# Optimization experiments

Hardware: AMD Instinct MI355X
Metric: run time of the kernel (lower is better)

The kernel has to match this reference:

```python
import jax, jax.numpy as jnp
import numpy as np

N, E, G = 20000, 320000, 64
IN_DIM, HID, HEADS, NCLS = 512, 256, 2, 10
EPS = 1e-5
SLOPE = 0.2


def setup_inputs() -> dict:
    key = jax.random.key(0)
    ks = jax.random.split(key, 24)
    s = 0.02
    inp = {
        "feat": jax.random.normal(ks[0], (N, IN_DIM), jnp.float32),
        "src": jax.random.randint(ks[1], (E,), 0, N, jnp.int32),
        "dst": jax.random.randint(ks[2], (E,), 0, N, jnp.int32),
        "graph_ids": jnp.sort(jax.random.randint(ks[3], (N,), 0, G, jnp.int32)),
        # GATv2Conv params (fc_src, fc_dst, attn)
        "W_src": jax.random.normal(ks[4], (IN_DIM, HEADS * HID), jnp.float32) * s,
        "b_src": jnp.zeros((HEADS * HID,), jnp.float32),
        "W_dst": jax.random.normal(ks[5], (IN_DIM, HEADS * HID), jnp.float32) * s,
        "b_dst": jnp.zeros((HEADS * HID,), jnp.float32),
        "attn": jax.random.normal(ks[6], (HEADS, HID), jnp.float32) * s,
        # skip_lin: input_dim -> 2*hidden
        "W_skip": jax.random.normal(ks[7], (IN_DIM, 2 * HID), jnp.float32) * s,
        "b_skip": jnp.zeros((2 * HID,), jnp.float32),
        # bn1 affine
        "gamma": jnp.ones((2 * HID,), jnp.float32),
        "beta": jnp.zeros((2 * HID,), jnp.float32),
        # dim_reducer
        "W_red": jax.random.normal(ks[8], (2 * HID, HID), jnp.float32) * s,
        "b_red": jnp.zeros((HID,), jnp.float32),
        # attention-pool gate Linear(hidden, 1)
        "w_gate": jax.random.normal(ks[9], (HID, 1), jnp.float32) * s,
        "b_gate": jnp.zeros((1,), jnp.float32),
        # classifier MLP
        "W1": jax.random.normal(ks[10], (HID, HID // 2), jnp.float32) * s,
        "b1": jnp.zeros((HID // 2,), jnp.float32),
        "W2": jax.random.normal(ks[11], (HID // 2, NCLS), jnp.float32) * s,
        "b2": jnp.zeros((NCLS,), jnp.float32),
    }
    return inp


def _gatv2(feat, src, dst, W_src, b_src, W_dst, b_dst, attn):
    # feat_src/feat_dst: [N, H, D]
    fs = (feat @ W_src + b_src).reshape(N, HEADS, HID)
    fd = (feat @ W_dst + b_dst).reshape(N, HEADS, HID)
    fs_e = fs[src]                               # [E, H, D]
    m = jax.nn.leaky_relu(fs_e + fd[dst], SLOPE)  # [E, H, D]
    e = jnp.einsum("ehd,hd->eh", m, attn)         # [E, H]
    # edge softmax grouped by destination node
    e_max = jax.ops.segment_max(e, dst, num_segments=N)          # [N, H]
    e_exp = jnp.exp(e - e_max[dst])                               # [E, H]
    denom = jax.ops.segment_sum(e_exp, dst, num_segments=N)      # [N, H]
    alpha = e_exp / denom[dst]                                    # [E, H]
    out = jax.ops.segment_sum(alpha[:, :, None] * fs_e, dst, num_segments=N)
    return out  # [N, H, D]; zero rows for zero in-degree nodes


def reference(feat, src, dst, graph_ids, W_src, b_src, W_dst, b_dst, attn,
              W_skip, b_skip, gamma, beta, W_red, b_red, w_gate, b_gate,
              W1, b1, W2, b2):
    h1 = jax.nn.elu(_gatv2(feat, src, dst, W_src, b_src, W_dst, b_dst, attn))
    h1 = h1.reshape(N, HEADS * HID)
    h1 = h1 + (feat @ W_skip + b_skip)
    # BatchNorm1d (training-mode batch statistics, biased variance)
    mu = jnp.mean(h1, axis=0)
    var = jnp.mean((h1 - mu) ** 2, axis=0)
    h1 = (h1 - mu) * jax.lax.rsqrt(var + EPS) * gamma + beta
    hr = h1 @ W_red + b_red                      # [N, HID]
    # GlobalAttentionPooling: segment softmax of gate scores over each graph
    gate = hr @ w_gate + b_gate                  # [N, 1]
    g_max = jax.ops.segment_max(gate, graph_ids, num_segments=G)
    g_exp = jnp.exp(gate - g_max[graph_ids])
    g_den = jax.ops.segment_sum(g_exp, graph_ids, num_segments=G)
    a = g_exp / g_den[graph_ids]                 # [N, 1]
    h_g = jax.ops.segment_sum(a * hr, graph_ids, num_segments=G)  # [G, HID]
    # classifier (dropout = identity at inference)
    return jax.nn.relu(h_g @ W1 + b1) @ W2 + b2  # [G, NCLS]
```

## Files before the change

### kernel.cpp

```cpp
#include <hip/hip_runtime.h>
#include <math.h>

#define N_NODES 20000
#define N_EDGES 320000
#define N_GRAPH 64
#define IN_DIM  512
#define HID     256
#define F2      512
#define EPS_BN  1e-5f
#define SLOPE   0.2f
#define SCAN_BLOCKS 79
#define N_RT    157
#define RT_PAD  20096

#define SF_BLOCKS   5024
#define SW_BLOCKS   1024
#define INIT_BLOCKS 79
#define HIST_BLOCKS 1250
#define PREP_BLOCKS (SF_BLOCKS + SW_BLOCKS + INIT_BLOCKS + HIST_BLOCKS)
#define TRIPLE_BLOCKS 1920

typedef unsigned short u16;
typedef __attribute__((ext_vector_type(8))) short bf16x8;
typedef __attribute__((ext_vector_type(4))) float floatx4;
typedef _Float16 f16;
typedef __attribute__((ext_vector_type(2))) f16 f16x2;

__device__ __forceinline__ u16 bf_hi(float x) {
    unsigned int u = __float_as_uint(x);
    return (u16)((u + 0x7fffu + ((u >> 16) & 1u)) >> 16);
}
__device__ __forceinline__ float bf_val(u16 h) {
    return __uint_as_float((unsigned int)h << 16);
}
__device__ __forceinline__ f16x2 h2_from_u32(unsigned int u) {
    return __builtin_bit_cast(f16x2, u);
}
__device__ __forceinline__ unsigned int u32_from_h2(f16x2 h) {
    return __builtin_bit_cast(unsigned int, h);
}

__device__ __forceinline__ void gload16(const u16* g, u16* l) {
    __builtin_amdgcn_global_load_lds(
        (const __attribute__((address_space(1))) void*)g,
        (__attribute__((address_space(3))) void*)l, 16, 0, 0);
}

__global__ __launch_bounds__(256) void prep_kernel(
    const float* __restrict__ feat, u16* __restrict__ Fhi,
    const float* __restrict__ Ws, const float* __restrict__ Wd,
    const float* __restrict__ Wk, const float* __restrict__ Wr,
    u16* __restrict__ Whi, u16* __restrict__ Wlo,
    const int* __restrict__ dst, int* __restrict__ counts,
    int* __restrict__ cursor,
    float* __restrict__ stats, float* __restrict__ h_gnum,
    float* __restrict__ gden, float* __restrict__ gate) {
    __shared__ float t[32][33];
    int b = blockIdx.x;
    int tid = threadIdx.x;
    if (b < SF_BLOCKS) {
        int i = b * 256 + tid;
        size_t base = (size_t)i * 8;
        if (i >= N_NODES * IN_DIM / 8) {
            *(uint4*)(Fhi + base) = make_uint4(0, 0, 0, 0);
            return;
        }
        float4 x0 = *(const float4*)(feat + base);
        float4 x1 = *(const float4*)(feat + base + 4);
        float xs[8] = {x0.x, x0.y, x0.z, x0.w, x1.x, x1.y, x1.z, x1.w};
        union { u16 s[8]; uint4 v; } h;
#pragma unroll
        for (int j = 0; j < 8; j++) h.s[j] = bf_hi(xs[j]);
        *(uint4*)(Fhi + base) = h.v;
    } else if (b < SF_BLOCKS + SW_BLOCKS) {
        int bb = b - SF_BLOCKS;
        int kx = bb & 15, ny = (bb >> 4) & 15, w = bb >> 8;
        int ncols = (w == 3) ? 256 : 512;
        int n0 = ny * 32;
        if (n0 >= ncols) return;
        const float* W = (w == 0) ? Ws : ((w == 1) ? Wd : ((w == 2) ? Wk : Wr));
        size_t obase = (size_t)w * 512 * 512;
        int k0 = kx * 32;
        int tx = tid & 31, ty = tid >> 5;
#pragma unroll
        for (int i = 0; i < 4; i++)
            t[ty * 4 + i][tx] = W[(size_t)(k0 + ty * 4 + i) * ncols + n0 + tx];
        __syncthreads();
#pragma unroll
        for (int i = 0; i < 4; i++) {
            float x = t[tx][ty * 4 + i];
            u16 hh = bf_hi(x);
            size_t o = obase + (size_t)(n0 + ty * 4 + i) * 512 + k0 + tx;
            Whi[o] = hh;
            Wlo[o] = bf_hi(x - bf_val(hh));
        }
    } else if (b < SF_BLOCKS + SW_BLOCKS + INIT_BLOCKS) {
        int i = (b - SF_BLOCKS - SW_BLOCKS) * 256 + tid;
        if (i < N_NODES) { cursor[i] = 0; gate[i] = 0.f; }
        if (i < 1024) stats[i] = 0.f;
        if (i < N_GRAPH * HID) h_gnum[i] = 0.f;
        if (i < N_GRAPH) gden[i] = 0.f;
    } else {
        int e = (b - SF_BLOCKS - SW_BLOCKS - INIT_BLOCKS) * 256 + tid;
        if (e < N_EDGES) atomicAdd(&counts[dst[e]], 1);
    }
}

__global__ __launch_bounds__(256) void gemm_mfma_triple(
    const u16* __restrict__ Fhi, const u16* __restrict__ Wthi,
    const float* __restrict__ b_src, const float* __restrict__ b_dst,
    const float* __restrict__ b_skip,
    u16* __restrict__ FS16, u16* __restrict__ FD16,
    u16* __restrict__ h1hi, u16* __restrict__ h1lo,
    const int* __restrict__ counts, int* __restrict__ row_ptr,
    int* __restrict__ bsum) {
    __shared__ u16 S[2][2][8192];
    int b = blockIdx.x;
    int tid = threadIdx.x;
    if (b >= TRIPLE_BLOCKS) {
        int* buf = (int*)&S[0][0][0];
        int bb = b - TRIPLE_BLOCKS;
        int i = bb * 256 + tid;
        buf[tid] = (i < N_NODES) ? counts[i] : 0;
        __syncthreads();
        for (int off = 1; off < 256; off <<= 1) {
            int t = (tid >= off) ? buf[tid - off] : 0;
            __syncthreads();
            buf[tid] += t;
            __syncthreads();
        }
        if (i < N_NODES) row_ptr[i + 1] = buf[tid];
        if (tid == 255) bsum[bb] = buf[255];
        return;
    }
    int xcd = b & 7, slot = b >> 3;
    int rt = (slot / 12) * 8 + xcd;
    if (rt >= N_RT) return;
    int cw = slot % 12;
    int w_idx = cw >> 2;
    int col0 = (cw & 3) * 128;
    int row0 = rt * 128;
    int lane = tid & 63, wave = tid >> 6;
    int wm = (wave & 1) * 64, wn = (wave >> 1) * 64;
    int quad = lane >> 4, l16 = lane & 15;

    int lrow = lane >> 3;
    int kswz = ((lane & 7) ^ lrow) << 3;
    const u16* aS = Fhi + (size_t)(row0 + wave * 32 + lrow) * 512 + kswz;
    const u16* bS = Wthi + (size_t)w_idx * 512 * 512 +
                    (size_t)(col0 + wave * 32 + lrow) * 512 + kswz;

#define STAGE(buf, kk)                                                        \
    do {                                                                      \
        gload16(aS + (size_t)(kk) * 64,         &S[buf][0][(wave * 4 + 0) * 512]); \
        gload16(bS + (size_t)(kk) * 64,         &S[buf][1][(wave * 4 + 0) * 512]); \
        gload16(aS + 4096 + (size_t)(kk) * 64,  &S[buf][0][(wave * 4 + 1) * 512]); \
        gload16(bS + 4096 + (size_t)(kk) * 64,  &S[buf][1][(wave * 4 + 1) * 512]); \
        gload16(aS + 8192 + (size_t)(kk) * 64,  &S[buf][0][(wave * 4 + 2) * 512]); \
        gload16(bS + 8192 + (size_t)(kk) * 64,  &S[buf][1][(wave * 4 + 2) * 512]); \
        gload16(aS + 12288 + (size_t)(kk) * 64, &S[buf][0][(wave * 4 + 3) * 512]); \
        gload16(bS + 12288 + (size_t)(kk) * 64, &S[buf][1][(wave * 4 + 3) * 512]); \
    } while (0)

    int kx8 = (l16 & 7) << 3;
    int oS0 = (quad * 8) ^ kx8;
    int offA = (wm + l16) * 64;
    int offB = (wn + l16) * 64;

    floatx4 acc[4][4];
#pragma unroll
    for (int i = 0; i < 4; i++)
#pragma unroll
        for (int j = 0; j < 4; j++) acc[i][j] = (floatx4){0.f, 0.f, 0.f, 0.f};

    STAGE(0, 0);
    __syncthreads();

#pragma unroll
    for (int kk = 0; kk < 8; kk++) {
        if (kk < 7) STAGE((kk + 1) & 1, kk + 1);
        const u16* A = &S[kk & 1][0][0];
        const u16* B = &S[kk & 1][1][0];
        bf16x8 bv[4][2];
#pragma unroll
        for (int nt = 0; nt < 4; nt++) {
            bv[nt][0] = *(const bf16x8*)&B[offB + nt * 1024 + oS0];
            bv[nt][1] = *(const bf16x8*)&B[offB + nt * 1024 + (oS0 ^ 32)];
        }
#pragma unroll
        for (int mt = 0; mt < 4; mt++) {
            bf16x8 a0 = *(const bf16x8*)&A[offA + mt * 1024 + oS0];
            bf16x8 a1 = *(const bf16x8*)&A[offA + mt * 1024 + (oS0 ^ 32)];
#pragma unroll
            for (int nt = 0; nt < 4; nt++) {
                acc[mt][nt] = __builtin_amdgcn_mfma_f32_16x16x32_bf16(
                    bv[nt][0], a0, acc[mt][nt], 0, 0, 0);
                acc[mt][nt] = __builtin_amdgcn_mfma_f32_16x16x32_bf16(
                    bv[nt][1], a1, acc[mt][nt], 0, 0, 0);
            }
        }
        __syncthreads();
    }
#undef STAGE

    const float* bias = (w_idx == 0) ? b_src : ((w_idx == 1) ? b_dst : b_skip);
    float4 b4[4];
#pragma unroll
    for (int wt = 0; wt < 4; wt++)
        b4[wt] = *(const float4*)(bias + col0 + wn + wt * 16 + quad * 4);

    u16* C = &S[0][0][0];
#pragma unroll
    for (int ft = 0; ft < 4; ft++) {
        int r = wm + ft * 16 + l16;
        int rx = r & 7;
#pragma unroll
        for (int wt = 0; wt < 4; wt++) {
            int cb = wn + wt * 16 + quad * 4;
            int off = r * 128 + (((cb >> 3) ^ rx) << 3) + (cb & 4);
            float v0 = acc[ft][wt][0] + b4[wt].x;
            float v1 = acc[ft][wt][1] + b4[wt].y;
            float v2 = acc[ft][wt][2] + b4[wt].z;
            float v3 = acc[ft][wt][3] + b4[wt].w;
            if (w_idx <= 1) {
                f16x2 p0; p0[0] = (f16)v0; p0[1] = (f16)v1;
                f16x2 p1; p1[0] = (f16)v2; p1[1] = (f16)v3;
                uint2 wv;
                wv.x = u32_from_h2(p0);
                wv.y = u32_from_h2(p1);
                *(uint2*)&C[off] = wv;
            } else {
                u16 h0 = bf_hi(v0), h1_ = bf_hi(v1), h2 = bf_hi(v2), h3 = bf_hi(v3);
                uint2 wv;
                wv.x = (unsigned)h0 | ((unsigned)h1_ << 16);
                wv.y = (unsigned)h2 | ((unsigned)h3 << 16);
                *(uint2*)&C[off] = wv;
                uint2 lv;
                lv.x = (unsigned)bf_hi(v0 - bf_val(h0)) | ((unsigned)bf_hi(v1 - bf_val(h1_)) << 16);
                lv.y = (unsigned)bf_hi(v2 - bf_val(h2)) | ((unsigned)bf_hi(v3 - bf_val(h3)) << 16);
                *(uint2*)&C[16384 + off] = lv;
            }
        }
    }
    __syncthreads();
    {
        int tr = tid >> 4;
        int tc = tid & 15;
        u16* outp = (w_idx == 0) ? FS16 : ((w_idx == 1) ? FD16 : h1hi);
#pragma unroll
        for (int i = 0; i < 8; i++) {
            int r = i * 16 + tr;
            int m = row0 + r;
            int loff = r * 128 + ((tc ^ (r & 7)) << 3);
            uint4 v = *(const uint4*)&C[loff];
            if (m < N_NODES) {
                *(uint4*)(outp + (size_t)m * 512 + col0 + tc * 8) = v;
                if (w_idx == 2) {
                    uint4 vl = *(const uint4*)&C[16384 + loff];
                    *(uint4*)(h1lo + (size_t)m * 512 + col0 + tc * 8) = vl;
                }
            }
        }
    }
}

__global__ __launch_bounds__(256) void scan_fixup_kernel(
    const int* __restrict__ bsum, int* __restrict__ row_ptr) {
    __shared__ int red[256];
    int b = blockIdx.x, tid = threadIdx.x;
    red[tid] = (tid < b) ? bsum[tid] : 0;
    __syncthreads();
    for (int off = 128; off > 0; off >>= 1) {
        if (tid < off) red[tid] += red[tid + off];
        __syncthreads();
    }
    int offset = red[0];
    int i = b * 256 + tid;
    if (i < N_NODES) row_ptr[i + 1] += offset;
    if (b == 0 && tid == 0) row_ptr[0] = 0;
}

__global__ void scatter_kernel(const int* __restrict__ src, const int* __restrict__ dst,
                               const int* __restrict__ row_ptr,
                               int* __restrict__ cursor, int* __restrict__ csr_src) {
    int e = blockIdx.x * blockDim.x + threadIdx.x;
    if (e < N_EDGES) {
        int d = dst[e];
        int pos = atomicAdd(&cursor[d], 1);
        csr_src[row_ptr[d] + pos] = src[e];
    }
}

__global__ __launch_bounds__(128) void edge_fused_kernel(
    const u16* __restrict__ FS16, const u16* __restrict__ FD16,
    const float* __restrict__ attn, const int* __restrict__ csr_src,
    const int* __restrict__ row_ptr,
    u16* __restrict__ h1hi, u16* __restrict__ h1lo) {
    int tid = threadIdx.x;
    int lane = tid & 63, wave = tid >> 6;
    int n = blockIdx.x * 2 + wave;
    int beg = row_ptr[n], end = row_ptr[n + 1];

    f16x2 fd2[4], aw2[4];
    {
        uint4 q = *(const uint4*)(FD16 + (size_t)n * 512 + 8 * lane);
        fd2[0] = h2_from_u32(q.x); fd2[1] = h2_from_u32(q.y);
        fd2[2] = h2_from_u32(q.z); fd2[3] = h2_from_u32(q.w);
        float4 a0 = *(const float4*)(attn + 8 * lane);
        float4 a1 = *(const float4*)(attn + 8 * lane + 4);
        aw2[0][0] = (f16)a0.x; aw2[0][1] = (f16)a0.y;
        aw2[1][0] = (f16)a0.z; aw2[1][1] = (f16)a0.w;
        aw2[2][0] = (f16)a1.x; aw2[2][1] = (f16)a1.y;
        aw2[3][0] = (f16)a1.z; aw2[3][1] = (f16)a1.w;
    }

    const f16x2 sl2 = {(f16)SLOPE, (f16)SLOPE};
    float acc[8] = {0.f, 0.f, 0.f, 0.f, 0.f, 0.f, 0.f, 0.f};
    float den = 0.f;
    const u16* FSb = FS16 + 8 * lane;

    int j = beg;
    for (; j + 3 < end; j += 4) {
        int s0 = csr_src[j];
        int s1 = csr_src[j + 1];
        int s2 = csr_src[j + 2];
        int s3 = csr_src[j + 3];
        uint4 q0 = *(const uint4*)(FSb + (size_t)s0 * 512);
        uint4 q1 = *(const uint4*)(FSb + (size_t)s1 * 512);
        uint4 q2 = *(const uint4*)(FSb + (size_t)s2 * 512);
        uint4 q3 = *(const uint4*)(FSb + (size_t)s3 * 512);
        f16x2 f0[4], f1[4], f2[4], f3[4];
        f0[0] = h2_from_u32(q0.x); f0[1] = h2_from_u32(q0.y);
        f0[2] = h2_from_u32(q0.z); f0[3] = h2_from_u32(q0.w);
        f1[0] = h2_from_u32(q1.x); f1[1] = h2_from_u32(q1.y);
        f1[2] = h2_from_u32(q1.z); f1[3] = h2_from_u32(q1.w);
        f2[0] = h2_from_u32(q2.x); f2[1] = h2_from_u32(q2.y);
        f2[2] = h2_from_u32(q2.z); f2[3] = h2_from_u32(q2.w);
        f3[0] = h2_from_u32(q3.x); f3[1] = h2_from_u32(q3.y);
        f3[2] = h2_from_u32(q3.z); f3[3] = h2_from_u32(q3.w);
        float p0 = 0.f, p1 = 0.f, p2 = 0.f, p3 = 0.f;
#pragma unroll
        for (int k = 0; k < 4; k++) {
            f16x2 sm0 = f0[k] + fd2[k];
            p0 = __builtin_amdgcn_fdot2(
                __builtin_elementwise_max(sm0, sm0 * sl2), aw2[k], p0, false);
            f16x2 sm1 = f1[k] + fd2[k];
            p1 = __builtin_amdgcn_fdot2(
                __builtin_elementwise_max(sm1, sm1 * sl2), aw2[k], p1, false);
            f16x2 sm2 = f2[k] + fd2[k];
            p2 = __builtin_amdgcn_fdot2(
                __builtin_elementwise_max(sm2, sm2 * sl2), aw2[k], p2, false);
            f16x2 sm3 = f3[k] + fd2[k];
            p3 = __builtin_amdgcn_fdot2(
                __builtin_elementwise_max(sm3, sm3 * sl2), aw2[k], p3, false);
        }
#pragma unroll
        for (int off = 16; off > 0; off >>= 1) {
            p0 += __shfl_xor(p0, off, 64);
            p1 += __shfl_xor(p1, off, 64);
            p2 += __shfl_xor(p2, off, 64);
            p3 += __shfl_xor(p3, off, 64);
        }
        float e0 = __expf(p0);
        float e1 = __expf(p1);
        float e2 = __expf(p2);
        float e3 = __expf(p3);
#pragma unroll
        for (int k = 0; k < 4; k++) {
            acc[2 * k]     += e0 * (float)f0[k][0] + e1 * (float)f1[k][0]
                            + e2 * (float)f2[k][0] + e3 * (float)f3[k][0];
            acc[2 * k + 1] += e0 * (float)f0[k][1] + e1 * (float)f1[k][1]
                            + e2 * (float)f2[k][1] + e3 * (float)f3[k][1];
        }
        den += (e0 + e1) + (e2 + e3);
    }
    for (; j < end; j++) {
        int s = csr_src[j];
        uint4 q = *(const uint4*)(FSb + (size_t)s * 512);
        f16x2 f2v[4];
        f2v[0] = h2_from_u32(q.x); f2v[1] = h2_from_u32(q.y);
        f2v[2] = h2_from_u32(q.z); f2v[3] = h2_from_u32(q.w);
        float p = 0.f;
#pragma unroll
        for (int k = 0; k < 4; k++) {
            f16x2 sm = f2v[k] + fd2[k];
            p = __builtin_amdgcn_fdot2(
                __builtin_elementwise_max(sm, sm * sl2), aw2[k], p, false);
        }
#pragma unroll
        for (int off = 16; off > 0; off >>= 1) p += __shfl_xor(p, off, 64);
        float ex = __expf(p);
#pragma unroll
        for (int k = 0; k < 4; k++) {
            acc[2 * k]     += ex * (float)f2v[k][0];
            acc[2 * k + 1] += ex * (float)f2v[k][1];
        }
        den += ex;
    }

    float inv = den > 0.f ? 1.f / den : 0.f;
    size_t base = (size_t)n * 512 + 8 * lane;
    union { u16 s[8]; uint4 v; } qh, ql;
    qh.v = *(const uint4*)(h1hi + base);
    ql.v = *(const uint4*)(h1lo + base);
#pragma unroll
    for (int k = 0; k < 8; k++) {
        float skip = bf_val(qh.s[k]) + bf_val(ql.s[k]);
        float x = acc[k] * inv;
        x = x > 0.f ? x : expm1f(x);
        float y = x + skip;
        u16 hh = bf_hi(y);
        qh.s[k] = hh;
        ql.s[k] = bf_hi(y - bf_val(hh));
    }
    *(uint4*)(h1hi + base) = qh.v;
    *(uint4*)(h1lo + base) = ql.v;
}

__global__ __launch_bounds__(256) void bn_stats_kernel(const u16* __restrict__ h1hi,
                                                       float* __restrict__ stats,
                                                       int rows_per_block) {
    int tid = threadIdx.x;
    int r0 = blockIdx.x * rows_per_block;
    int r1 = min(r0 + rows_per_block, N_NODES);
    float s0 = 0.f, q0 = 0.f, s1 = 0.f, q1 = 0.f;
    for (int r = r0; r < r1; r++) {
        float a = bf_val(h1hi[(size_t)r * F2 + tid]);
        float b = bf_val(h1hi[(size_t)r * F2 + 256 + tid]);
        s0 += a; q0 += a * a;
        s1 += b; q1 += b * b;
    }
    atomicAdd(&stats[tid], s0);
    atomicAdd(&stats[256 + tid], s1);
    atomicAdd(&stats[512 + tid], q0);
    atomicAdd(&stats[512 + 256 + tid], q1);
}

__global__ __launch_bounds__(256) void bn_fold_kernel(
    const float* __restrict__ stats, const float* __restrict__ gamma,
    const float* __restrict__ beta,
    const u16* __restrict__ Whi3, const u16* __restrict__ Wlo3,
    const float* __restrict__ b_red,
    u16* __restrict__ Wphi, u16* __restrict__ Wplo, float* __restrict__ bias2) {
    __shared__ float sScale[512], sShift[512];
    __shared__ float red[256];
    int n = blockIdx.x, tid = threadIdx.x;
    for (int c = tid; c < 512; c += 256) {
        float mu = stats[c] / (float)N_NODES;
        float var = stats[512 + c] / (float)N_NODES - mu * mu;
        float sc = gamma[c] * rsqrtf(var + EPS_BN);
        sScale[c] = sc;
        sShift[c] = beta[c] - mu * sc;
    }
    __syncthreads();
    float part = 0.f;
    for (int k = tid; k < 512; k += 256) {
        size_t o = (size_t)n * 512 + k;
        float w = bf_val(Whi3[o]) + bf_val(Wlo3[o]);
        part += sShift[k] * w;
        float wp = w * sScale[k];
        u16 hh = bf_hi(wp);
        Wphi[o] = hh;
        Wplo[o] = bf_hi(wp - bf_val(hh));
    }
    red[tid] = part; __syncthreads();
    for (int off = 128; off > 0; off >>= 1) {
        if (tid < off) red[tid] += red[tid + off];
        __syncthreads();
    }
    if (tid == 0) bias2[n] = b_red[n] + red[0];
}

__global__ __launch_bounds__(256) void gemm_mfma_red(
    const u16* __restrict__ Ahi, const u16* __restrict__ Alo,
    const u16* __restrict__ Bhi, const u16* __restrict__ Blo,
    const float* __restrict__ bias2, const float* __restrict__ wg,
    float* __restrict__ hr, float* __restrict__ gate) {
    __shared__ float CS[128 * 128];
    u16* AsHi = (u16*)CS;
    u16* AsLo = (u16*)CS + 128 * 40;
    int tid = threadIdx.x;
    int row0 = blockIdx.x * 128;
    int col0 = blockIdx.y * 128;
    int lane = tid & 63, wave = tid >> 6;
    int wm = (wave & 1) * 64, wn = (wave >> 1) * 64;
    int quad = lane >> 4, l16 = lane & 15;

    int sr = tid >> 1, sh = (tid & 1) * 16;
    int grow = row0 + sr;
    bool ok = grow < N_NODES;
    u16* sH = &AsHi[sr * 40 + sh];
    u16* sL = &AsLo[sr * 40 + sh];

    const u16* bPh[4];
    const u16* bPl[4];
#pragma unroll
    for (int nt = 0; nt < 4; nt++) {
        size_t o = (size_t)(col0 + wn + nt * 16 + l16) * 512 + quad * 8;
        bPh[nt] = Bhi + o;
        bPl[nt] = Blo + o;
    }

    floatx4 acc[4][4];
#pragma unroll
    for (int i = 0; i < 4; i++)
#pragma unroll
        for (int j = 0; j < 4; j++) acc[i][j] = (floatx4){0.f, 0.f, 0.f, 0.f};

    for (int k0 = 0; k0 < 512; k0 += 32) {
        uint4 h0 = make_uint4(0, 0, 0, 0), h1v = h0, l0 = h0, l1 = h0;
        if (ok) {
            const u16* g = Ahi + (size_t)grow * 512 + k0 + sh;
            const u16* gl = Alo + (size_t)grow * 512 + k0 + sh;
            h0 = *(const uint4*)(g);
            h1v = *(const uint4*)(g + 8);
            l0 = *(const uint4*)(gl);
            l1 = *(const uint4*)(gl + 8);
        }
        union { uint4 u; bf16x8 v; } bh[4], bl[4];
#pragma unroll
        for (int nt = 0; nt < 4; nt++) {
            bh[nt].u = *(const uint4*)(bPh[nt] + k0);
            bl[nt].u = *(const uint4*)(bPl[nt] + k0);
        }
        __syncthreads();
        *(uint4*)(sH + 0) = h0;
        *(uint4*)(sH + 8) = h1v;
        *(uint4*)(sL + 0) = l0;
        *(uint4*)(sL + 8) = l1;
        __syncthreads();
#pragma unroll
        for (int mt = 0; mt < 4; mt++) {
            int me = (wm + mt * 16 + l16) * 40 + quad * 8;
            bf16x8 ah = *(const bf16x8*)&AsHi[me];
            bf16x8 al = *(const bf16x8*)&AsLo[me];
#pragma unroll
            for (int nt = 0; nt < 4; nt++) {
                acc[mt][nt] = __builtin_amdgcn_mfma_f32_16x16x32_bf16(bh[nt].v, ah, acc[mt][nt], 0, 0, 0);
                acc[mt][nt] = __builtin_amdgcn_mfma_f32_16x16x32_bf16(bl[nt].v, ah, acc[mt][nt], 0, 0, 0);
                acc[mt][nt] = __builtin_amdgcn_mfma_f32_16x16x32_bf16(bh[nt].v, al, acc[mt][nt], 0, 0, 0);
            }
        }
    }
    __syncthreads();

    float4 b4[4], w4[4];
#pragma unroll
    for (int wt = 0; wt < 4; wt++) {
        int nb = col0 + wn + wt * 16 + quad * 4;
        b4[wt] = *(const float4*)(bias2 + nb);
        w4[wt] = *(const float4*)(wg + nb);
    }
#pragma unroll
    for (int ft = 0; ft < 4; ft++) {
        int r = wm + ft * 16 + l16;
        int m = row0 + r;
        bool ok2 = m < N_NODES;
        float g = 0.f;
#pragma unroll
        for (int wt = 0; wt < 4; wt++) {
            int cb = wn + wt * 16 + quad * 4;
            float4 v;
            v.x = acc[ft][wt][0] + b4[wt].x;
            v.y = acc[ft][wt][1] + b4[wt].y;
            v.z = acc[ft][wt][2] + b4[wt].z;
            v.w = acc[ft][wt][3] + b4[wt].w;
            g += v.x * w4[wt].x + v.y * w4[wt].y + v.z * w4[wt].z + v.w * w4[wt].w;
            *(float4*)&CS[r * 128 + (((cb >> 2) ^ (r & 7)) << 2)] = v;
        }
        g += __shfl_xor(g, 16, 64);
        g += __shfl_xor(g, 32, 64);
        if (ok2 && lane < 16) atomicAdd(&gate[m], g);
    }
    __syncthreads();
    {
        int trr = tid >> 5;
        int tc = tid & 31;
#pragma unroll
        for (int it = 0; it < 16; it++) {
            int r = it * 8 + trr;
            int m = row0 + r;
            if (m < N_NODES) {
                float4 v = *(const float4*)&CS[r * 128 + ((tc ^ (r & 7)) << 2)];
                *(float4*)(hr + (size_t)m * HID + col0 + tc * 4) = v;
            }
        }
    }
}

__device__ __forceinline__ int lower_bound_dev(const int* a, int n, int v) {
    int lo = 0, hi = n;
    while (lo < hi) {
        int mid = (lo + hi) >> 1;
        if (a[mid] < v) lo = mid + 1; else hi = mid;
    }
    return lo;
}

__global__ __launch_bounds__(256) void pool_partial_kernel(
    const float* __restrict__ hr, const float* __restrict__ gate,
    const int* __restrict__ gids, float* __restrict__ h_gnum,
    float* __restrict__ gden) {
    int b = blockIdx.x;
    int g = b >> 3, part = b & 7;
    int tid = threadIdx.x;
    int start = lower_bound_dev(gids, N_NODES, g);
    int end = lower_bound_dev(gids, N_NODES, g + 1);
    int span = end - start;
    int p_beg = start + (span * part) / 8;
    int p_end = start + (span * (part + 1)) / 8;
    if (p_beg >= p_end) return;
    __shared__ float wa[256];
    __shared__ float red[256];
    float acc = 0.f, denacc = 0.f;
    for (int cbeg = p_beg; cbeg < p_end; cbeg += 256) {
        int c = min(256, p_end - cbeg);
        float e = 0.f;
        if (tid < c) { e = expf(gate[cbeg + tid]); wa[tid] = e; }
        red[tid] = (tid < c) ? e : 0.f;
        __syncthreads();
        for (int off = 128; off > 0; off >>= 1) {
            if (tid < off) red[tid] += red[tid + off];
            __syncthreads();
        }
        denacc += red[0];
        for (int i = 0; i < c; i++) acc += wa[i] * hr[(size_t)(cbeg + i) * HID + tid];
        __syncthreads();
    }
    atomicAdd(&h_gnum[g * HID + tid], acc);
    if (tid == 0) atomicAdd(&gden[g], denacc);
}

__global__ __launch_bounds__(128) void classifier_kernel(
    const float* __restrict__ h_gnum, const float* __restrict__ gden,
    const float* __restrict__ W1, const float* __restrict__ b1,
    const float* __restrict__ W2, const float* __restrict__ b2,
    float* __restrict__ out) {
    int g = blockIdx.x;
    int tid = threadIdx.x;
    __shared__ float hg[256];
    __shared__ float z1[128];
    float d = gden[g];
    float invd = d > 0.f ? 1.f / d : 0.f;
    hg[tid] = h_gnum[g * HID + tid] * invd;
    hg[tid + 128] = h_gnum[g * HID + tid + 128] * invd;
    __syncthreads();
    float a = b1[tid];
#pragma unroll 8
    for (int k = 0; k < 256; k++) a += hg[k] * W1[k * 128 + tid];
    z1[tid] = a > 0.f ? a : 0.f;
    __syncthreads();
    if (tid < 10) {
        float o = b2[tid];
#pragma unroll 8
        for (int j = 0; j < 128; j++) o += z1[j] * W2[j * 10 + tid];
        out[g * 10 + tid] = o;
    }
}

extern "C" void kernel_launch(void* const* d_in, const int* in_sizes, int n_in,
                              void* d_out, int out_size, void* d_ws, size_t ws_size,
                              hipStream_t stream) {
    const float* feat   = (const float*)d_in[0];
    const int*   src    = (const int*)d_in[1];
    const int*   dst    = (const int*)d_in[2];
    const int*   gids   = (const int*)d_in[3];
    const float* W_src  = (const float*)d_in[4];
    const float* b_src  = (const float*)d_in[5];
    const float* W_dst  = (const float*)d_in[6];
    const float* b_dst  = (const float*)d_in[7];
    const float* attn   = (const float*)d_in[8];
    const float* W_skip = (const float*)d_in[9];
    const float* b_skip = (const float*)d_in[10];
    const float* gamma  = (const float*)d_in[11];
    const float* beta   = (const float*)d_in[12];
    const float* W_red  = (const float*)d_in[13];
    const float* b_red  = (const float*)d_in[14];
    const float* w_gate = (const float*)d_in[15];
    const float* W1     = (const float*)d_in[17];
    const float* b1     = (const float*)d_in[18];
    const float* W2     = (const float*)d_in[19];
    const float* b2     = (const float*)d_in[20];
    float* out = (float*)d_out;

    char* p = (char*)d_ws;
    auto alloc = [&](size_t bytes) -> char* {
        char* r = p;
        p += (bytes + 255) & ~(size_t)255;
        return r;
    };
    u16*   FS16     = (u16*)alloc((size_t)N_NODES * F2 * 2);
    u16*   FD16     = (u16*)alloc((size_t)N_NODES * F2 * 2);
    u16*   h1hi     = (u16*)alloc((size_t)N_NODES * F2 * 2);
    u16*   h1lo     = (u16*)alloc((size_t)N_NODES * F2 * 2);
    float* gate     = (float*)alloc((size_t)N_NODES * 4);
    float* stats    = (float*)alloc(1024 * 4);
    float* bias2    = (float*)alloc(256 * 4);
    float* h_gnum   = (float*)alloc((size_t)N_GRAPH * HID * 4);
    float* gden     = (float*)alloc((size_t)N_GRAPH * 4);
    int* counts     = (int*)alloc((size_t)N_NODES * 4);
    int* row_ptr    = (int*)alloc((size_t)(N_NODES + 1) * 4);
    int* cursor     = (int*)alloc((size_t)N_NODES * 4);
    int* csr_src    = (int*)alloc((size_t)N_EDGES * 4);
    int* bsum       = (int*)alloc((size_t)SCAN_BLOCKS * 4);
    u16* Fhi        = (u16*)alloc((size_t)RT_PAD * IN_DIM * 2);
    u16* Wthi       = (u16*)alloc((size_t)4 * 512 * 512 * 2);
    u16* Wtlo       = (u16*)alloc((size_t)4 * 512 * 512 * 2);
    u16* Wphi       = (u16*)alloc((size_t)HID * 512 * 2);
    u16* Wplo       = (u16*)alloc((size_t)HID * 512 * 2);
    float* hr = (float*)Fhi;
    (void)ws_size; (void)in_sizes; (void)n_in; (void)out_size;

    const size_t WSZ = (size_t)512 * 512;

    hipMemsetAsync(counts, 0, (size_t)N_NODES * 4, stream);

    prep_kernel<<<PREP_BLOCKS, 256, 0, stream>>>(
        feat, Fhi, W_src, W_dst, W_skip, W_red, Wthi, Wtlo,
        dst, counts, cursor, stats, h_gnum, gden, gate);

    gemm_mfma_triple<<<TRIPLE_BLOCKS + SCAN_BLOCKS, 256, 0, stream>>>(
        Fhi, Wthi, b_src, b_dst, b_skip, FS16, FD16, h1hi, h1lo,
        counts, row_ptr, bsum);

    scan_fixup_kernel<<<SCAN_BLOCKS, 256, 0, stream>>>(bsum, row_ptr);
    scatter_kernel<<<(N_EDGES + 255) / 256, 256, 0, stream>>>(src, dst, row_ptr, cursor, csr_src);

    edge_fused_kernel<<<N_NODES / 2, 128, 0, stream>>>(
        FS16, FD16, attn, csr_src, row_ptr, h1hi, h1lo);

    bn_stats_kernel<<<500, 256, 0, stream>>>(h1hi, stats, 40);
    bn_fold_kernel<<<HID, 256, 0, stream>>>(
        stats, gamma, beta, Wthi + 3 * WSZ, Wtlo + 3 * WSZ, b_red, Wphi, Wplo, bias2);

    dim3 g256((N_NODES + 127) / 128, 2);
    gemm_mfma_red<<<g256, 256, 0, stream>>>(
        h1hi, h1lo, Wphi, Wplo, bias2, w_gate, hr, gate);

    pool_partial_kernel<<<N_GRAPH * 8, 256, 0, stream>>>(hr, gate, gids, h_gnum, gden);

    classifier_kernel<<<N_GRAPH, 128, 0, stream>>>(h_gnum, gden, W1, b1, W2, b2, out);
}
```

Measured before the change: 361.3 us.

## Fuse attention pooling into reduction GEMM epilogue and widen edge kernel blocks

The reduction GEMM now covers all 256 output columns in one 512-thread block per 128-row tile. It computes the gate score fully in shared memory, then accumulates exp(gate)-weighted rows into per-graph shared partial sums before flushing them to global memory with atomics. This removes the hr and gate intermediate arrays and the separate pool_partial kernel, which reread hr. The softmax max-subtraction is skipped, relying on gate values staying small, and the grid shrinks to 157 blocks, which may underfill the GPU. The edge kernel also moves from 2 to 4 waves per block.

```diff
diff --git a/kernel.cpp b/kernel.cpp
--- a/kernel.cpp
+++ b/kernel.cpp
@@ -54,7 +54,7 @@
     const int* __restrict__ dst, int* __restrict__ counts,
     int* __restrict__ cursor,
     float* __restrict__ stats, float* __restrict__ h_gnum,
-    float* __restrict__ gden, float* __restrict__ gate) {
+    float* __restrict__ gden) {
     __shared__ float t[32][33];
     int b = blockIdx.x;
     int tid = threadIdx.x;
@@ -96,7 +96,7 @@
         }
     } else if (b < SF_BLOCKS + SW_BLOCKS + INIT_BLOCKS) {
         int i = (b - SF_BLOCKS - SW_BLOCKS) * 256 + tid;
-        if (i < N_NODES) { cursor[i] = 0; gate[i] = 0.f; }
+        if (i < N_NODES) cursor[i] = 0;
         if (i < 1024) stats[i] = 0.f;
         if (i < N_GRAPH * HID) h_gnum[i] = 0.f;
         if (i < N_GRAPH) gden[i] = 0.f;
@@ -291,14 +291,14 @@
     }
 }
 
-__global__ __launch_bounds__(128) void edge_fused_kernel(
+__global__ __launch_bounds__(256) void edge_fused_kernel(
     const u16* __restrict__ FS16, const u16* __restrict__ FD16,
     const float* __restrict__ attn, const int* __restrict__ csr_src,
     const int* __restrict__ row_ptr,
     u16* __restrict__ h1hi, u16* __restrict__ h1lo) {
     int tid = threadIdx.x;
     int lane = tid & 63, wave = tid >> 6;
-    int n = blockIdx.x * 2 + wave;
+    int n = blockIdx.x * 4 + wave;
     int beg = row_ptr[n], end = row_ptr[n + 1];
 
     f16x2 fd2[4], aw2[4];
@@ -471,22 +471,28 @@
     if (tid == 0) bias2[n] = b_red[n] + red[0];
 }
 
-__global__ __launch_bounds__(256) void gemm_mfma_red(
+__global__ __launch_bounds__(512) void gemm_mfma_red(
     const u16* __restrict__ Ahi, const u16* __restrict__ Alo,
     const u16* __restrict__ Bhi, const u16* __restrict__ Blo,
     const float* __restrict__ bias2, const float* __restrict__ wg,
-    float* __restrict__ hr, float* __restrict__ gate) {
-    __shared__ float CS[128 * 128];
-    u16* AsHi = (u16*)CS;
-    u16* AsLo = (u16*)CS + 128 * 40;
+    const int* __restrict__ gids,
+    float* __restrict__ h_gnum, float* __restrict__ gden) {
+    __shared__ u16 AsHi[128 * 40];
+    __shared__ u16 AsLo[128 * 40];
+    __shared__ float gacc[128];
+    __shared__ float pacc[8][256];
+    __shared__ float dacc[8];
     int tid = threadIdx.x;
     int row0 = blockIdx.x * 128;
-    int col0 = blockIdx.y * 128;
     int lane = tid & 63, wave = tid >> 6;
     int wm = (wave & 1) * 64, wn = (wave >> 1) * 64;
     int quad = lane >> 4, l16 = lane & 15;
 
-    int sr = tid >> 1, sh = (tid & 1) * 16;
+    if (tid < 128) gacc[tid] = 0.f;
+    if (tid < 8) dacc[tid] = 0.f;
+    for (int i = tid; i < 8 * 256; i += 512) ((float*)pacc)[i] = 0.f;
+
+    int sr = tid >> 2, sh = (tid & 3) * 8;
     int grow = row0 + sr;
     bool ok = grow < N_NODES;
     u16* sH = &AsHi[sr * 40 + sh];
@@ -496,7 +502,7 @@
     const u16* bPl[4];
 #pragma unroll
     for (int nt = 0; nt < 4; nt++) {
-        size_t o = (size_t)(col0 + wn + nt * 16 + l16) * 512 + quad * 8;
+        size_t o = (size_t)(wn + nt * 16 + l16) * 512 + quad * 8;
         bPh[nt] = Bhi + o;
         bPl[nt] = Blo + o;
     }
@@ -508,14 +514,10 @@
         for (int j = 0; j < 4; j++) acc[i][j] = (floatx4){0.f, 0.f, 0.f, 0.f};
 
     for (int k0 = 0; k0 < 512; k0 += 32) {
-        uint4 h0 = make_uint4(0, 0, 0, 0), h1v = h0, l0 = h0, l1 = h0;
+        uint4 h0 = make_uint4(0, 0, 0, 0), l0 = h0;
         if (ok) {
-            const u16* g = Ahi + (size_t)grow * 512 + k0 + sh;
-            const u16* gl = Alo + (size_t)grow * 512 + k0 + sh;
-            h0 = *(const uint4*)(g);
-            h1v = *(const uint4*)(g + 8);
-            l0 = *(const uint4*)(gl);
-            l1 = *(const uint4*)(gl + 8);
+            h0 = *(const uint4*)(Ahi + (size_t)grow * 512 + k0 + sh);
+            l0 = *(const uint4*)(Alo + (size_t)grow * 512 + k0 + sh);
         }
         union { uint4 u; bf16x8 v; } bh[4], bl[4];
 #pragma unroll
@@ -524,10 +526,8 @@
             bl[nt].u = *(const uint4*)(bPl[nt] + k0);
         }
         __syncthreads();
-        *(uint4*)(sH + 0) = h0;
-        *(uint4*)(sH + 8) = h1v;
-        *(uint4*)(sL + 0) = l0;
-        *(uint4*)(sL + 8) = l1;
+        *(uint4*)sH = h0;
+        *(uint4*)sL = l0;
         __syncthreads();
 #pragma unroll
         for (int mt = 0; mt < 4; mt++) {
@@ -542,93 +542,74 @@
             }
         }
     }
-    __syncthreads();
 
     float4 b4[4], w4[4];
 #pragma unroll
     for (int wt = 0; wt < 4; wt++) {
-        int nb = col0 + wn + wt * 16 + quad * 4;
+        int nb = wn + wt * 16 + quad * 4;
         b4[wt] = *(const float4*)(bias2 + nb);
         w4[wt] = *(const float4*)(wg + nb);
     }
 #pragma unroll
     for (int ft = 0; ft < 4; ft++) {
         int r = wm + ft * 16 + l16;
-        int m = row0 + r;
-        bool ok2 = m < N_NODES;
         float g = 0.f;
 #pragma unroll
         for (int wt = 0; wt < 4; wt++) {
-            int cb = wn + wt * 16 + quad * 4;
             float4 v;
             v.x = acc[ft][wt][0] + b4[wt].x;
             v.y = acc[ft][wt][1] + b4[wt].y;
             v.z = acc[ft][wt][2] + b4[wt].z;
             v.w = acc[ft][wt][3] + b4[wt].w;
             g += v.x * w4[wt].x + v.y * w4[wt].y + v.z * w4[wt].z + v.w * w4[wt].w;
-            *(float4*)&CS[r * 128 + (((cb >> 2) ^ (r & 7)) << 2)] = v;
         }
         g += __shfl_xor(g, 16, 64);
         g += __shfl_xor(g, 32, 64);
-        if (ok2 && lane < 16) atomicAdd(&gate[m], g);
+        if (quad == 0) atomicAdd(&gacc[r], g);
     }
     __syncthreads();
-    {
-        int trr = tid >> 5;
-        int tc = tid & 31;
-#pragma unroll
-        for (int it = 0; it < 16; it++) {
-            int r = it * 8 + trr;
-            int m = row0 + r;
-            if (m < N_NODES) {
-                float4 v = *(const float4*)&CS[r * 128 + ((tc ^ (r & 7)) << 2)];
-                *(float4*)(hr + (size_t)m * HID + col0 + tc * 4) = v;
+
+    int g0 = gids[row0];
+#pragma unroll
+    for (int ft = 0; ft < 4; ft++) {
+        int r = wm + ft * 16 + l16;
+        int m = row0 + r;
+        if (m >= N_NODES) continue;
+        float wgt = __expf(gacc[r]);
+        int d = gids[m] - g0;
+        if (d < 8) {
+            if ((wave >> 1) == 0 && quad == 0) atomicAdd(&dacc[d], wgt);
+#pragma unroll
+            for (int wt = 0; wt < 4; wt++) {
+                int nb = wn + wt * 16 + quad * 4;
+                atomicAdd(&pacc[d][nb + 0], wgt * (acc[ft][wt][0] + b4[wt].x));
+                atomicAdd(&pacc[d][nb + 1], wgt * (acc[ft][wt][1] + b4[wt].y));
+                atomicAdd(&pacc[d][nb + 2], wgt * (acc[ft][wt][2] + b4[wt].z));
+                atomicAdd(&pacc[d][nb + 3], wgt * (acc[ft][wt][3] + b4[wt].w));
             }
-        }
-    }
-}
-
-__device__ __forceinline__ int lower_bound_dev(const int* a, int n, int v) {
-    int lo = 0, hi = n;
-    while (lo < hi) {
-        int mid = (lo + hi) >> 1;
-        if (a[mid] < v) lo = mid + 1; else hi = mid;
-    }
-    return lo;
-}
-
-__global__ __launch_bounds__(256) void pool_partial_kernel(
-    const float* __restrict__ hr, const float* __restrict__ gate,
-    const int* __restrict__ gids, float* __restrict__ h_gnum,
-    float* __restrict__ gden) {
-    int b = blockIdx.x;
-    int g = b >> 3, part = b & 7;
-    int tid = threadIdx.x;
-    int start = lower_bound_dev(gids, N_NODES, g);
-    int end = lower_bound_dev(gids, N_NODES, g + 1);
-    int span = end - start;
-    int p_beg = start + (span * part) / 8;
-    int p_end = start + (span * (part + 1)) / 8;
-    if (p_beg >= p_end) return;
-    __shared__ float wa[256];
-    __shared__ float red[256];
-    float acc = 0.f, denacc = 0.f;
-    for (int cbeg = p_beg; cbeg < p_end; cbeg += 256) {
-        int c = min(256, p_end - cbeg);
-        float e = 0.f;
-        if (tid < c) { e = expf(gate[cbeg + tid]); wa[tid] = e; }
-        red[tid] = (tid < c) ? e : 0.f;
-        __syncthreads();
-        for (int off = 128; off > 0; off >>= 1) {
-            if (tid < off) red[tid] += red[tid + off];
-            __syncthreads();
-        }
-        denacc += red[0];
-        for (int i = 0; i < c; i++) acc += wa[i] * hr[(size_t)(cbeg + i) * HID + tid];
-        __syncthreads();
-    }
-    atomicAdd(&h_gnum[g * HID + tid], acc);
-    if (tid == 0) atomicAdd(&gden[g], denacc);
+        } else {
+            int gg = gids[m];
+            if ((wave >> 1) == 0 && quad == 0) atomicAdd(&gden[gg], wgt);
+#pragma unroll
+            for (int wt = 0; wt < 4; wt++) {
+                int nb = wn + wt * 16 + quad * 4;
+                atomicAdd(&h_gnum[gg * HID + nb + 0], wgt * (acc[ft][wt][0] + b4[wt].x));
+                atomicAdd(&h_gnum[gg * HID + nb + 1], wgt * (acc[ft][wt][1] + b4[wt].y));
+                atomicAdd(&h_gnum[gg * HID + nb + 2], wgt * (acc[ft][wt][2] + b4[wt].z));
+                atomicAdd(&h_gnum[gg * HID + nb + 3], wgt * (acc[ft][wt][3] + b4[wt].w));
+            }
+        }
+    }
+    __syncthreads();
+
+    int mlast = min(row0 + 127, N_NODES - 1);
+    int span = gids[mlast] - g0;
+    if (span > 7) span = 7;
+    for (int i = tid; i < (span + 1) * 256; i += 512) {
+        int d = i >> 8, c = i & 255;
+        atomicAdd(&h_gnum[(g0 + d) * HID + c], pacc[d][c]);
+    }
+    if (tid <= span) atomicAdd(&gden[g0 + tid], dacc[tid]);
 }
 
 __global__ __launch_bounds__(128) void classifier_kernel(
@@ -693,7 +674,6 @@
     u16*   FD16     = (u16*)alloc((size_t)N_NODES * F2 * 2);
     u16*   h1hi     = (u16*)alloc((size_t)N_NODES * F2 * 2);
     u16*   h1lo     = (u16*)alloc((size_t)N_NODES * F2 * 2);
-    float* gate     = (float*)alloc((size_t)N_NODES * 4);
     float* stats    = (float*)alloc(1024 * 4);
     float* bias2    = (float*)alloc(256 * 4);
     float* h_gnum   = (float*)alloc((size_t)N_GRAPH * HID * 4);
@@ -708,7 +688,6 @@
     u16* Wtlo       = (u16*)alloc((size_t)4 * 512 * 512 * 2);
     u16* Wphi       = (u16*)alloc((size_t)HID * 512 * 2);
     u16* Wplo       = (u16*)alloc((size_t)HID * 512 * 2);
-    float* hr = (float*)Fhi;
     (void)ws_size; (void)in_sizes; (void)n_in; (void)out_size;
 
     const size_t WSZ = (size_t)512 * 512;
@@ -717,7 +696,7 @@
 
     prep_kernel<<<PREP_BLOCKS, 256, 0, stream>>>(
         feat, Fhi, W_src, W_dst, W_skip, W_red, Wthi, Wtlo,
-        dst, counts, cursor, stats, h_gnum, gden, gate);
+        dst, counts, cursor, stats, h_gnum, gden);
 
     gemm_mfma_triple<<<TRIPLE_BLOCKS + SCAN_BLOCKS, 256, 0, stream>>>(
         Fhi, Wthi, b_src, b_dst, b_skip, FS16, FD16, h1hi, h1lo,
@@ -726,18 +705,15 @@
     scan_fixup_kernel<<<SCAN_BLOCKS, 256, 0, stream>>>(bsum, row_ptr);
     scatter_kernel<<<(N_EDGES + 255) / 256, 256, 0, stream>>>(src, dst, row_ptr, cursor, csr_src);
 
-    edge_fused_kernel<<<N_NODES / 2, 128, 0, stream>>>(
+    edge_fused_kernel<<<N_NODES / 4, 256, 0, stream>>>(
         FS16, FD16, attn, csr_src, row_ptr, h1hi, h1lo);
 
     bn_stats_kernel<<<500, 256, 0, stream>>>(h1hi, stats, 40);
     bn_fold_kernel<<<HID, 256, 0, stream>>>(
         stats, gamma, beta, Wthi + 3 * WSZ, Wtlo + 3 * WSZ, b_red, Wphi, Wplo, bias2);
 
-    dim3 g256((N_NODES + 127) / 128, 2);
-    gemm_mfma_red<<<g256, 256, 0, stream>>>(
-        h1hi, h1lo, Wphi, Wplo, bias2, w_gate, hr, gate);
-
-    pool_partial_kernel<<<N_GRAPH * 8, 256, 0, stream>>>(hr, gate, gids, h_gnum, gden);
+    gemm_mfma_red<<<N_RT, 512, 0, stream>>>(
+        h1hi, h1lo, Wphi, Wplo, bias2, w_gate, gids, h_gnum, gden);
 
     classifier_kernel<<<N_GRAPH, 128, 0, stream>>>(h_gnum, gden, W1, b1, W2, b2, out);
 }
```

Result: slower. 390.9 us (+8.2%).
